# Kernel optimization log

Measured on AMD Instinct MI355X. Metric: run time of the kernel, lower is better.

The kernel has to match this reference:

```python
import jax, jax.numpy as jnp
import numpy as np

B, P, F, E, H, V = 128, 196, 2048, 512, 1024, 10000
TMAX = 30  # max(captions_len) - 1 decode steps
BN_EPS = 1e-5


def setup_inputs() -> dict:
    key = jax.random.key(0)
    ks = jax.random.split(key, 14)
    encoder_feat = jax.random.normal(ks[0], (B, P, F), jnp.float32)
    gt_captions = jax.random.randint(ks[1], (B, TMAX + 1), 0, V, dtype=jnp.int32)
    lens = jax.random.randint(ks[2], (B,), 2, TMAX + 2, dtype=jnp.int32)
    lens = lens.at[0].set(TMAX + 1)
    captions_len = jnp.sort(lens)[::-1]  # sorted descending, as the torch slicing assumes
    embedding = jax.random.uniform(ks[3], (V, E), jnp.float32, -0.1, 0.1)
    W_init = jax.random.normal(ks[4], (E, F), jnp.float32) * np.sqrt(2.0 / F)
    b_init = jnp.zeros((E,), jnp.float32)
    bn_gamma = jnp.ones((E,), jnp.float32)
    bn_beta = jnp.zeros((E,), jnp.float32)
    s = 1.0 / np.sqrt(H)
    W_ih = jax.random.uniform(ks[5], (4 * H, E), jnp.float32, -s, s)
    b_ih = jax.random.uniform(ks[6], (4 * H,), jnp.float32, -s, s)
    W_hh = jax.random.uniform(ks[7], (4 * H, H), jnp.float32, -s, s)
    b_hh = jax.random.uniform(ks[8], (4 * H,), jnp.float32, -s, s)
    W_fc = jax.random.normal(ks[9], (V, H), jnp.float32) * np.sqrt(2.0 / H)
    b_fc = jnp.zeros((V,), jnp.float32)
    return {
        'encoder_feat': encoder_feat, 'gt_captions': gt_captions, 'captions_len': captions_len,
        'embedding': embedding, 'W_init': W_init, 'b_init': b_init,
        'bn_gamma': bn_gamma, 'bn_beta': bn_beta,
        'W_ih': W_ih, 'b_ih': b_ih, 'W_hh': W_hh, 'b_hh': b_hh,
        'W_fc': W_fc, 'b_fc': b_fc,
    }


def _lstm_cell(h, c, x, W_ih, b_ih, W_hh, b_hh):
    # PyTorch LSTMCell: gates = x W_ih^T + b_ih + h W_hh^T + b_hh, order [i, f, g, o]
    gates = x @ W_ih.T + b_ih + h @ W_hh.T + b_hh
    i, f, g, o = jnp.split(gates, 4, axis=-1)
    c_new = jax.nn.sigmoid(f) * c + jax.nn.sigmoid(i) * jnp.tanh(g)
    h_new = jax.nn.sigmoid(o) * jnp.tanh(c_new)
    return h_new, c_new


def reference(encoder_feat, gt_captions, captions_len, embedding, W_init, b_init,
              bn_gamma, bn_beta, W_ih, b_ih, W_hh, b_hh, W_fc, b_fc):
    batch = encoder_feat.shape[0]
    hidden = W_hh.shape[1]
    # t == 0: image feature -> sigmoid(linear) -> BatchNorm1d (eval: rm=0, rv=1)
    feat = encoder_feat.mean(axis=1)                      # [B, F]
    x0 = jax.nn.sigmoid(feat @ W_init.T + b_init)         # [B, E]
    x0 = bn_gamma * (x0 / jnp.sqrt(1.0 + BN_EPS)) + bn_beta
    h0 = jnp.zeros((batch, hidden), x0.dtype)
    c0 = jnp.zeros((batch, hidden), x0.dtype)
    h, c = _lstm_cell(h0, c0, x0, W_ih, b_ih, W_hh, b_hh)
    # decode steps t = 1..TMAX over ground-truth token embeddings
    emb = embedding[gt_captions[:, :TMAX]]                # [B, T, E]
    xs = jnp.swapaxes(emb, 0, 1)                          # [T, B, E]

    def step(carry, x_t):
        h, c = carry
        h, c = _lstm_cell(h, c, x_t, W_ih, b_ih, W_hh, b_hh)
        preds = h @ W_fc.T + b_fc                         # [B, V]
        return (h, c), preds

    _, preds = jax.lax.scan(step, (h, c), xs)             # [T, B, V]
    preds = jnp.swapaxes(preds, 0, 1)                     # [B, T, V]
    # rows beyond batch_size_t were never written in torch (zeros tensor) -> mask
    mask = jnp.arange(TMAX)[None, :] < (captions_len - 1)[:, None]  # [B, T]
    return jnp.where(mask[:, :, None], preds, 0.0)
```

## Files before the change

### kernel.cpp

```cpp
#include <hip/hip_runtime.h>
#include <math.h>

typedef __bf16 bf16;
typedef __bf16 bf16x8 __attribute__((ext_vector_type(8)));
typedef __bf16 bf16x4 __attribute__((ext_vector_type(4)));
typedef float f32x4 __attribute__((ext_vector_type(4)));

#define MFMA_B16(a,b,c) __builtin_amdgcn_mfma_f32_16x16x32_bf16((a),(b),(c),0,0,0)

constexpr int TMAXc = 30;
constexpr int Bc = 128, Pc = 196, Fc = 2048, Ec = 512, Hc = 1024, Vc = 10000;
constexpr int G4c = 4 * Hc;
constexpr int NSTEP = TMAXc + 1;
constexpr int MALLc = NSTEP * Bc;
constexpr int MOUTc = TMAXc * Bc;
constexpr int NBLK = 256;

__device__ __forceinline__ float fsigm(float x){
  return __fdividef(1.0f, 1.0f + __expf(-x));
}
__device__ __forceinline__ float ftanh(float x){
  return 1.0f - __fdividef(2.0f, __expf(2.0f*x) + 1.0f);
}
__device__ __forceinline__ float sel4(float a, float b, float c, float d, int i){
  float x = (i & 1) ? b : a;
  float y = (i & 1) ? d : c;
  return (i & 2) ? y : x;
}

__device__ __forceinline__ void gll16(const void* g, void* l){
  __builtin_amdgcn_global_load_lds((const __attribute__((address_space(1))) void*)g,
                                   (__attribute__((address_space(3))) void*)l, 16, 0, 0);
}

__device__ __forceinline__ void wt16(bf16* p, bf16x8 v){
  asm volatile("global_store_dwordx4 %0, %1, off sc0 sc1" :: "v"(p), "v"(v) : "memory");
}

__device__ __forceinline__ int aldf(int* f){
  return __hip_atomic_load(f, __ATOMIC_RELAXED, __HIP_MEMORY_SCOPE_AGENT);
}

__device__ __forceinline__ void waitflag(int* f, int tgt){
  long long t0 = __builtin_amdgcn_s_memrealtime();
  while (aldf(f) < tgt) {
    __builtin_amdgcn_s_sleep(1);
    if (__builtin_amdgcn_s_memrealtime() - t0 > 100000) break;
  }
}

__device__ __forceinline__ void waitflags4(int* F, int& f1, int& f2, int& f3){
  long long t0 = __builtin_amdgcn_s_memrealtime();
  for (;;) {
    int f0 = aldf(F + 0);
    f1 = aldf(F + 1);
    f2 = aldf(F + 2);
    f3 = aldf(F + 3);
    if (f0 >= 32) break;
    __builtin_amdgcn_s_sleep(1);
    if (__builtin_amdgcn_s_memrealtime() - t0 > 100000) break;
  }
}


__global__ void mean_kernel(const float* __restrict__ enc, bf16* __restrict__ feat){
  int blk = blockIdx.x, b = blk >> 1, half = blk & 1;
  int f0 = half*1024 + threadIdx.x*4;
  const float* p = enc + (size_t)b*Pc*Fc + f0;
  float4 s = {0.f,0.f,0.f,0.f};
  #pragma unroll 4
  for (int q = 0; q < Pc; ++q) {
    float4 v = *(const float4*)(p + (size_t)q*Fc);
    s.x += v.x; s.y += v.y; s.z += v.z; s.w += v.w;
  }
  const float r = 1.0f/(float)Pc;
  bf16x4 o = { (bf16)(s.x*r), (bf16)(s.y*r), (bf16)(s.z*r), (bf16)(s.w*r) };
  *(bf16x4*)&feat[b*Fc + f0] = o;
}

__global__ void conv_kernel(const float* __restrict__ src, bf16* __restrict__ dst, int n4){
  int i = blockIdx.x*256 + threadIdx.x;
  if (i >= n4) return;
  float4 v = ((const float4*)src)[i];
  bf16x4 o = { (bf16)v.x, (bf16)v.y, (bf16)v.z, (bf16)v.w };
  *(bf16x4*)&dst[i*4] = o;
}

__global__ void permconv_ih(const float* __restrict__ W, bf16* __restrict__ Wp){
  int i = blockIdx.x*256 + threadIdx.x;
  if (i >= G4c*Ec/4) return;
  int i4 = i*4;
  int rp = i4 >> 9, k = i4 & 511;
  int g = rp & 3, j = rp >> 2;
  float4 v = *(const float4*)&W[(size_t)(g*Hc + j)*Ec + k];
  bf16x4 o = { (bf16)v.x, (bf16)v.y, (bf16)v.z, (bf16)v.w };
  *(bf16x4*)&Wp[i4] = o;
}

__global__ void permsplit_hh(const float* __restrict__ W, bf16* __restrict__ Whi, bf16* __restrict__ Wlo){
  int i = blockIdx.x*256 + threadIdx.x;
  if (i >= G4c*Hc/4) return;
  int i4 = i*4;
  int rp = i4 >> 10, k = i4 & 1023;
  int g = rp & 3, j = rp >> 2;
  float4 v = *(const float4*)&W[(size_t)(g*Hc + j)*Hc + k];
  bf16 h0=(bf16)v.x, h1=(bf16)v.y, h2=(bf16)v.z, h3=(bf16)v.w;
  bf16x4 hi = { h0, h1, h2, h3 };
  bf16x4 lo = { (bf16)(v.x-(float)h0), (bf16)(v.y-(float)h1), (bf16)(v.z-(float)h2), (bf16)(v.w-(float)h3) };
  *(bf16x4*)&Whi[i4] = hi;
  *(bf16x4*)&Wlo[i4] = lo;
}

__global__ void split_kernel(const float* __restrict__ W, bf16* __restrict__ Whi, bf16* __restrict__ Wlo, int n4){
  int i = blockIdx.x*256 + threadIdx.x;
  if (i >= n4) return;
  float4 v = ((const float4*)W)[i];
  bf16 h0=(bf16)v.x, h1=(bf16)v.y, h2=(bf16)v.z, h3=(bf16)v.w;
  bf16x4 hi = { h0, h1, h2, h3 };
  bf16x4 lo = { (bf16)(v.x-(float)h0), (bf16)(v.y-(float)h1), (bf16)(v.z-(float)h2), (bf16)(v.w-(float)h3) };
  *(bf16x4*)&Whi[i*4] = hi;
  *(bf16x4*)&Wlo[i*4] = lo;
}

__global__ void bcomb_kernel(const float* __restrict__ bih, const float* __restrict__ bhh, float* __restrict__ bc){
  int i = blockIdx.x*256 + threadIdx.x;
  if (i >= G4c) return;
  int g = i & 3, j = i >> 2;
  bc[i] = bih[g*Hc + j] + bhh[g*Hc + j];
}

__global__ void gather_kernel(const float* __restrict__ emb, const int* __restrict__ gt, bf16* __restrict__ X){
  int idx = blockIdx.x*256 + threadIdx.x;
  if (idx >= MOUTc*(Ec/4)) return;
  int r = idx >> 7, ei = (idx & 127) * 4;
  int s = (r >> 7) + 1, b = r & 127;
  int tok = gt[b*(TMAXc+1) + (s-1)];
  float4 v = *(const float4*)(emb + (size_t)tok*Ec + ei);
  bf16x4 o = { (bf16)v.x, (bf16)v.y, (bf16)v.z, (bf16)v.w };
  *(bf16x4*)&X[(size_t)(s*Bc + b)*Ec + ei] = o;
}

__global__ void build_ridx(const int* __restrict__ lens, int* __restrict__ meta){
  int i = blockIdx.x*256 + threadIdx.x;
  if (i >= MOUTc) return;
  int t = i >> 7, b = i & 127;
  int S = 0, R = 0;
  for (int bb = 0; bb < 128; ++bb) {
    int l = lens[bb] - 1;
    S += (t < l) ? t : l;
    R += l;
  }
  if (i == 0) meta[0] = R;
  if (i >= R) meta[1 + i] = 0;
  if (t < lens[b] - 1) meta[1 + S + b] = i;
}

__global__ void zerofill(const int* __restrict__ lens, float* __restrict__ out){
  int i = blockIdx.x*256 + threadIdx.x;
  if (i >= MOUTc*2500) return;
  int row = i / 2500, c4 = i - row*2500;
  int b = row / TMAXc, t = row - b*TMAXc;
  if (t >= lens[b] - 1) {
    float4 z = {0.f,0.f,0.f,0.f};
    *(float4*)(out + (size_t)row*Vc + c4*4) = z;
  }
}

__global__ __launch_bounds__(256, 2) void initA(
  const bf16* __restrict__ feat, const bf16* __restrict__ Wi, float* __restrict__ part)
{
  __shared__ alignas(16) bf16 sA[128*32], sB[128*32];
  int tid = threadIdx.x, lane = tid & 63, w = tid >> 6, wr = w >> 1, wc = w & 1;
  int nt = blockIdx.x & 3, kc = blockIdx.x >> 2;
  int n0 = nt*128;

  f32x4 acc[4][4] = {};
  for (int kt = kc*256; kt < kc*256 + 256; kt += 32) {
    #pragma unroll
    for (int is = 0; is < 2; ++is) {
      int p = tid*16 + is*4096;
      int r = p >> 6, c = (p & 63) >> 1;
      int ldsoff = w*512 + is*2048;
      gll16(feat + (size_t)r*Fc + kt + c, &sA[ldsoff]);
      gll16(Wi + (size_t)(n0 + r)*Fc + kt + c, &sB[ldsoff]);
    }
    __syncthreads();
    int koff = (lane >> 4) * 8;
    bf16x8 ah[4], bh[4];
    #pragma unroll
    for (int mi = 0; mi < 4; ++mi)
      ah[mi] = *(const bf16x8*)&sA[(wr*64 + mi*16 + (lane & 15))*32 + koff];
    #pragma unroll
    for (int ni = 0; ni < 4; ++ni)
      bh[ni] = *(const bf16x8*)&sB[(wc*64 + ni*16 + (lane & 15))*32 + koff];
    #pragma unroll
    for (int mi = 0; mi < 4; ++mi)
      #pragma unroll
      for (int ni = 0; ni < 4; ++ni)
        acc[mi][ni] = MFMA_B16(ah[mi], bh[ni], acc[mi][ni]);
    __syncthreads();
  }
  #pragma unroll
  for (int mi = 0; mi < 4; ++mi)
    #pragma unroll
    for (int ni = 0; ni < 4; ++ni) {
      int lrow = wr*64 + mi*16 + ((lane >> 4) << 2);
      int col = n0 + wc*64 + ni*16 + (lane & 15);
      #pragma unroll
      for (int j = 0; j < 4; ++j)
        part[((size_t)kc*128 + lrow + j)*512 + col] = acc[mi][ni][j];
    }
}

__global__ void initB(const float* __restrict__ part, const float* __restrict__ binit,
                      const float* __restrict__ gam, const float* __restrict__ bet,
                      bf16* __restrict__ Xall)
{
  int i = blockIdx.x*256 + threadIdx.x;
  if (i >= 128*512) return;
  int col = i & 511;
  float v = 0.f;
  #pragma unroll
  for (int kc = 0; kc < 8; ++kc) v += part[(size_t)kc*128*512 + i];
  const float rbn = rsqrtf(1.0f + 1e-5f);
  v = fsigm(v + binit[col]);
  v = gam[col]*(v*rbn) + bet[col];
  Xall[i] = (bf16)v;
}

__global__ __launch_bounds__(256, 2) void gemm_xg(
  const bf16* __restrict__ A, const bf16* __restrict__ B,
  int M, int N, int K, int mtiles,
  const float* __restrict__ p0, bf16* __restrict__ outb)
{
  constexpr int BK = 32;
  __shared__ alignas(16) bf16 sAh[128*BK], sBh[128*BK];

  int tid = threadIdx.x;
  int lane = tid & 63, w = tid >> 6, wr = w >> 1, wc = w & 1;
  int bid = blockIdx.x;
  {
    int nwg = gridDim.x, q = nwg >> 3, r = nwg & 7;
    int x = bid & 7, o = bid >> 3;
    bid = (x < r ? x*(q+1) : r*(q+1) + (x-r)*q) + o;
  }
  int nt = bid / mtiles, mt = bid - nt*mtiles;
  int m0 = mt*128, n0 = nt*128;

  int sr = (tid*16) >> 6;
  int gr0 = m0 + sr, gr1 = m0 + sr + 64;

  f32x4 acc[4][4] = {};

  for (int kt = 0; kt < K; kt += BK) {
    #pragma unroll
    for (int is = 0; is < 2; ++is) {
      int p = tid*16 + is*4096;
      int c = (p & 63) >> 1;
      int r = p >> 6;
      int ldsoff = w*512 + is*2048;
      int ga = is ? gr1 : gr0;
      gll16(A + (size_t)ga*K + kt + c, &sAh[ldsoff]);
      gll16(B + (size_t)(n0 + r)*K + kt + c, &sBh[ldsoff]);
    }
    __syncthreads();

    int koff = (lane >> 4) * 8;
    bf16x8 ah[4], bh[4];
    #pragma unroll
    for (int mi = 0; mi < 4; ++mi)
      ah[mi] = *(const bf16x8*)&sAh[(wr*64 + mi*16 + (lane & 15))*BK + koff];
    #pragma unroll
    for (int ni = 0; ni < 4; ++ni)
      bh[ni] = *(const bf16x8*)&sBh[(wc*64 + ni*16 + (lane & 15))*BK + koff];
    #pragma unroll
    for (int mi = 0; mi < 4; ++mi)
      #pragma unroll
      for (int ni = 0; ni < 4; ++ni)
        acc[mi][ni] = MFMA_B16(ah[mi], bh[ni], acc[mi][ni]);
    __syncthreads();
  }

  #pragma unroll
  for (int mi = 0; mi < 4; ++mi)
    #pragma unroll
    for (int ni = 0; ni < 4; ++ni) {
      int lrow = m0 + wr*64 + mi*16 + ((lane >> 4) << 2);
      int col = n0 + wc*64 + ni*16 + (lane & 15);
      #pragma unroll
      for (int j = 0; j < 4; ++j)
        outb[(size_t)(lrow + j)*G4c + col] = (bf16)(acc[mi][ni][j] + p0[col]);
    }
}


__global__ __launch_bounds__(256, 1) void lstm_persist(
  const bf16* __restrict__ Whi, const bf16* __restrict__ Wlo,
  const bf16* __restrict__ Xg,
  bf16* __restrict__ hCh, bf16* __restrict__ hCl,
  bf16* __restrict__ Hh, bf16* __restrict__ Hl,
  const bf16* __restrict__ WfcHi, const bf16* __restrict__ WfcLo,
  const float* __restrict__ bfc,
  const int* __restrict__ lens, const int* __restrict__ meta,
  float* __restrict__ outf,
  int* __restrict__ flg)
{
  extern __shared__ char sWc[];
  int tid = threadIdx.x, lane = tid & 63, w = tid >> 6;
  int bid = blockIdx.x;
  int strip = bid >> 1, rh = bid & 1;
  int pc0 = strip * 32;
  int row0 = rh * 64 + w * 16;
  int grp = strip >> 5;
  char* scr = sWc + 131072 + w*512;
  int* hallflg = flg + 256;
  int* tilectr = flg + 320;

  for (int ch = tid; ch < 4096; ch += 256) {
    int p = ch >> 7;
    int k = (ch & 127) * 8;
    int ni = p >> 4, bp = p & 15;
    int ks = k >> 5, kg = (k >> 3) & 3;
    int off = (((ks*2 + ni)*4 + kg)*16 + bp) * 16;
    bf16x8 vh = *(const bf16x8*)&Whi[(size_t)(pc0 + p)*Hc + k];
    bf16x8 vl = *(const bf16x8*)&Wlo[(size_t)(pc0 + p)*Hc + k];
    *(bf16x8*)(sWc + off) = vh;
    *(bf16x8*)(sWc + 65536 + off) = vl;
  }
  __syncthreads();

  int bp = lane & 15;
  int bk = (lane >> 4) << 3;
  int rbase = row0 + ((lane >> 4) << 2);
  int e = lane & 3;
  const char* sWhiB = sWc + lane*16;
  const char* sWloB = sWc + 65536 + lane*16;

  int Lh = lens[rh * 64];
  if (Lh > NSTEP) Lh = NSTEP;
  int lenv = lens[row0 + (lane & 15)] - 1;

  float creg[2] = {0.f, 0.f};
  float xgv[2][4];
  #pragma unroll
  for (int ni = 0; ni < 2; ++ni)
    #pragma unroll
    for (int j = 0; j < 4; ++j)
      xgv[ni][j] = (float)Xg[(size_t)(rbase + j)*G4c + pc0 + ni*16 + bp];

#define GATEQ(g, fg) do { if (s > 0) { \
    if (tid == 0 && (fg) < 32) waitflag(&flg[(s*2 + rh)*4 + (g)], 32); \
    __builtin_amdgcn_s_barrier(); \
    asm volatile("" ::: "memory"); } } while (0)

#define LOADQ(qh, ql, g) do { \
    _Pragma("unroll") \
    for (int i = 0; i < 8; ++i) { \
      qh[i] = *(const bf16x8*)(pah + ((g)*8 + i)*32); \
      ql[i] = *(const bf16x8*)(pal + ((g)*8 + i)*32); \
    } \
    asm volatile("" ::: "memory"); } while (0)

#define MFMAQ(qh, ql, g) do { \
    _Pragma("unroll") \
    for (int i = 0; i < 8; ++i) { \
      int ks = (g)*8 + i; \
      _Pragma("unroll") \
      for (int ni = 0; ni < 2; ++ni) { \
        bf16x8 bvh = *(const bf16x8*)(sWhiB + (ks*2 + ni)*1024); \
        bf16x8 bvl = *(const bf16x8*)(sWloB + (ks*2 + ni)*1024); \
        aHH[ni] = MFMA_B16(qh[i], bvh, aHH[ni]); \
        aHL[ni] = MFMA_B16(qh[i], bvl, aHL[ni]); \
        aLH[ni] = MFMA_B16(ql[i], bvh, aLH[ni]); \
      } \
    } } while (0)

  #pragma unroll 1
  for (int s = 0; s < Lh; ++s) {
    const bf16* pah = hCh + (size_t)s*Bc*Hc + (size_t)(row0 + bp)*Hc + bk;
    const bf16* pal = hCl + (size_t)s*Bc*Hc + (size_t)(row0 + bp)*Hc + bk;
    bf16* hwh = hCh + (size_t)(s+1)*Bc*Hc;
    bf16* hwl = hCl + (size_t)(s+1)*Bc*Hc;

    f32x4 aHH[2], aHL[2], aLH[2];
    #pragma unroll
    for (int ni = 0; ni < 2; ++ni) {
      #pragma unroll
      for (int j = 0; j < 4; ++j) aHH[ni][j] = xgv[ni][j];
      aHL[ni] = (f32x4){0.f,0.f,0.f,0.f};
      aLH[ni] = (f32x4){0.f,0.f,0.f,0.f};
    }

    bf16x8 qh0[8], ql0[8], qh1[8], ql1[8];
    int f1 = 32, f2 = 32, f3 = 32;

    if (s > 0) {
      if (tid == 0) waitflags4(&flg[(s*2 + rh)*4], f1, f2, f3);
      __builtin_amdgcn_s_barrier();
      asm volatile("" ::: "memory");
    }
    LOADQ(qh0, ql0, 0);
    GATEQ(1, f1); LOADQ(qh1, ql1, 1);
    MFMAQ(qh0, ql0, 0);
    GATEQ(2, f2); LOADQ(qh0, ql0, 2);
    MFMAQ(qh1, ql1, 1);
    GATEQ(3, f3); LOADQ(qh1, ql1, 3);
    MFMAQ(qh0, ql0, 2);
    MFMAQ(qh1, ql1, 3);

    #pragma unroll
    for (int ni = 0; ni < 2; ++ni) {
      float v0 = aHH[ni][0] + aHL[ni][0] + aLH[ni][0];
      float v1 = aHH[ni][1] + aHL[ni][1] + aLH[ni][1];
      float v2 = aHH[ni][2] + aHL[ni][2] + aLH[ni][2];
      float v3 = aHH[ni][3] + aHL[ni][3] + aLH[ni][3];
      float g0 = sel4(v0, v1, v2, v3, e);
      float g1 = __shfl_xor(sel4(v0, v1, v2, v3, e ^ 1), 1);
      float g2 = __shfl_xor(sel4(v0, v1, v2, v3, e ^ 2), 2);
      float g3 = __shfl_xor(sel4(v0, v1, v2, v3, e ^ 3), 3);
      float gI = sel4(g0, g1, g2, g3, e);
      float gF = sel4(g0, g1, g2, g3, e ^ 1);
      float gG = sel4(g0, g1, g2, g3, e ^ 2);
      float gO = sel4(g0, g1, g2, g3, e ^ 3);

      float co = creg[ni];
      float cn = fsigm(gF)*co + fsigm(gI)*ftanh(gG);
      float hn = fsigm(gO)*ftanh(cn);
      creg[ni] = cn;
      bf16 hhi = (bf16)hn;
      int r16 = ((lane >> 4) << 2) + e;
      int c8  = ni*4 + (bp >> 2);
      *(bf16*)(scr + (r16*8 + c8)*2) = hhi;
      *(bf16*)(scr + 256 + (r16*8 + c8)*2) = (bf16)(hn - (float)hhi);
    }

    asm volatile("s_waitcnt lgkmcnt(0)" ::: "memory");
    __builtin_amdgcn_sched_barrier(0);

    if (lane < 32) {
      int r = lane & 15, buf = lane >> 4;
      bf16x8 vv = *(const bf16x8*)(scr + buf*256 + r*16);
      bf16* dst = (buf ? hwl : hwh) + (size_t)(row0 + r)*Hc + strip*8;
      wt16(dst, vv);
    }

    __syncthreads();
    if (tid == 0 && s + 1 < Lh)
      __hip_atomic_fetch_add(&flg[((s+1)*2 + rh)*4 + grp], 1,
                             __ATOMIC_RELAXED, __HIP_MEMORY_SCOPE_AGENT);

    if (s > 0 && lane >= 32 && (s - 1) < lenv) {
      int r = lane & 15, buf = (lane >> 4) & 1;
      bf16x8 vv = *(const bf16x8*)(scr + buf*256 + r*16);
      wt16((buf ? Hl : Hh) + (size_t)((s-1)*Bc + row0 + r)*Hc + strip*8, vv);
    }
    if (s + 1 < Lh) {
      #pragma unroll
      for (int ni = 0; ni < 2; ++ni)
        #pragma unroll
        for (int j = 0; j < 4; ++j)
          xgv[ni][j] = (float)Xg[(size_t)((s+1)*Bc + rbase + j)*G4c + pc0 + ni*16 + bp];
    }

    __syncthreads();
    if (tid == 0 && s > 0)
      __hip_atomic_fetch_add(&hallflg[(s-1)*2 + rh], 1,
                             __ATOMIC_RELAXED, __HIP_MEMORY_SCOPE_AGENT);
  }
#undef GATEQ
#undef LOADQ
#undef MFMAQ

  if (tid == 0)
    for (int t = Lh - 1; t < TMAXc; ++t)
      __hip_atomic_fetch_add(&hallflg[t*2 + rh], 1,
                             __ATOMIC_RELAXED, __HIP_MEMORY_SCOPE_AGENT);

  __syncthreads();

  bf16* sAh2 = (bf16*)(sWc);
  bf16* sBh2 = (bf16*)(sWc + 32768);
  bf16* sAl2 = (bf16*)(sWc + 65536);
  bf16* sBl2 = (bf16*)(sWc + 98304);
  int* ctrl  = (int*)(sWc + 131072 + 2044);

  int R = meta[0];
  int mtilesFC = (R + 127) >> 7;
  int ntFC = mtilesFC * 79;
  int wr = w >> 1, wc2 = w & 1;

#define STAGE_FC(buf, kt) do { \
    _Pragma("unroll") \
    for (int is = 0; is < 2; ++is) { \
      int p = tid*16 + is*4096; \
      int c = (p & 63) >> 1; \
      int r = p >> 6; \
      int ldsoff = (buf)*4096 + w*512 + is*2048; \
      int ga = is ? gr1 : gr0; \
      int rb = n0 + r; if (rb > 9999) rb = 9999; \
      gll16(Hh + (size_t)ga*Hc + (kt) + c, &sAh2[ldsoff]); \
      gll16(WfcHi + (size_t)rb*Hc + (kt) + c, &sBh2[ldsoff]); \
      gll16(Hl + (size_t)ga*Hc + (kt) + c, &sAl2[ldsoff]); \
      gll16(WfcLo + (size_t)rb*Hc + (kt) + c, &sBl2[ldsoff]); \
    } } while (0)

  #pragma unroll 1
  for (;;) {
    if (tid == 0) ctrl[0] = __hip_atomic_fetch_add(tilectr, 1,
                               __ATOMIC_RELAXED, __HIP_MEMORY_SCOPE_AGENT);
    __syncthreads();
    int idx = ctrl[0];
    __syncthreads();
    if (idx >= ntFC) break;
    int mt = idx / 79, ntc = idx - mt*79;
    int m0 = mt*128, n0 = ntc*128;
    int last = m0 + 127; if (last >= R) last = R - 1;
    int tmax = meta[1 + last] >> 7;
    if (tid == 0) {
      waitflag(&hallflg[tmax*2 + 0], 128);
      waitflag(&hallflg[tmax*2 + 1], 128);
    }
    __builtin_amdgcn_s_barrier();
    asm volatile("" ::: "memory");

    int sr = (tid*16) >> 6;
    int gr0 = meta[1 + m0 + sr], gr1 = meta[1 + m0 + sr + 64];

    f32x4 acc[4][4] = {};

    STAGE_FC(0, 0);
    asm volatile("s_waitcnt vmcnt(0)" ::: "memory");
    __builtin_amdgcn_s_barrier();
    asm volatile("" ::: "memory");

    #pragma unroll 1
    for (int ks = 0; ks < 32; ++ks) {
      int buf = ks & 1;
      if (ks + 1 < 32) STAGE_FC(buf ^ 1, (ks+1)*32);

      int koff = (lane >> 4) * 8;
      int bb = buf*4096;
      bf16x8 ah[4], bh[4], al[4], bl[4];
      #pragma unroll
      for (int mi = 0; mi < 4; ++mi) {
        int rr = wr*64 + mi*16 + (lane & 15);
        ah[mi] = *(const bf16x8*)&sAh2[bb + rr*32 + koff];
        al[mi] = *(const bf16x8*)&sAl2[bb + rr*32 + koff];
      }
      #pragma unroll
      for (int ni = 0; ni < 4; ++ni) {
        int rr = wc2*64 + ni*16 + (lane & 15);
        bh[ni] = *(const bf16x8*)&sBh2[bb + rr*32 + koff];
        bl[ni] = *(const bf16x8*)&sBl2[bb + rr*32 + koff];
      }
      #pragma unroll
      for (int mi = 0; mi < 4; ++mi)
        #pragma unroll
        for (int ni = 0; ni < 4; ++ni) {
          acc[mi][ni] = MFMA_B16(ah[mi], bh[ni], acc[mi][ni]);
          acc[mi][ni] = MFMA_B16(ah[mi], bl[ni], acc[mi][ni]);
          acc[mi][ni] = MFMA_B16(al[mi], bh[ni], acc[mi][ni]);
        }

      asm volatile("s_waitcnt vmcnt(0)" ::: "memory");
      __builtin_amdgcn_s_barrier();
      asm volatile("" ::: "memory");
    }

    #pragma unroll
    for (int mi = 0; mi < 4; ++mi)
      #pragma unroll
      for (int ni = 0; ni < 4; ++ni) {
        int lrow = m0 + wr*64 + mi*16 + ((lane >> 4) << 2);
        int col = n0 + wc2*64 + ni*16 + (lane & 15);
        #pragma unroll
        for (int j = 0; j < 4; ++j) {
          int rr = lrow + j;
          if (rr < R && col < Vc) {
            int val = meta[1 + rr];
            int t = val >> 7, b = val & 127;
            outf[(size_t)b*(TMAXc*Vc) + (size_t)t*Vc + col] = acc[mi][ni][j] + bfc[col];
          }
        }
      }
  }
#undef STAGE_FC
}


extern "C" void kernel_launch(void* const* d_in, const int* in_sizes, int n_in,
                              void* d_out, int out_size, void* d_ws, size_t ws_size,
                              hipStream_t stream)
{
  const float* enc   = (const float*)d_in[0];
  const int*   gt    = (const int*)  d_in[1];
  const int*   lens  = (const int*)  d_in[2];
  const float* emb   = (const float*)d_in[3];
  const float* Winit = (const float*)d_in[4];
  const float* binit = (const float*)d_in[5];
  const float* gam   = (const float*)d_in[6];
  const float* bet   = (const float*)d_in[7];
  const float* Wih   = (const float*)d_in[8];
  const float* bih   = (const float*)d_in[9];
  const float* Whh   = (const float*)d_in[10];
  const float* bhh   = (const float*)d_in[11];
  const float* Wfc   = (const float*)d_in[12];
  const float* bfc   = (const float*)d_in[13];
  float* out = (float*)d_out;

  char* ws = (char*)d_ws;
  size_t off = 0;
  auto alloc = [&](size_t bytes) -> char* {
    char* p = ws + off;
    off += (bytes + 255) & ~(size_t)255;
    return p;
  };

  bf16* featB  = (bf16*)alloc((size_t)Bc*Fc*2);
  bf16* WinitB = (bf16*)alloc((size_t)Ec*Fc*2);
  bf16* WihpB  = (bf16*)alloc((size_t)G4c*Ec*2);
  bf16* WhhHi  = (bf16*)alloc((size_t)G4c*Hc*2);
  bf16* WhhLo  = (bf16*)alloc((size_t)G4c*Hc*2);
  bf16* WfcHi  = (bf16*)alloc((size_t)Vc*Hc*2);
  bf16* WfcLo  = (bf16*)alloc((size_t)Vc*Hc*2);
  float* bcomb = (float*)alloc((size_t)G4c*4);
  bf16* Xall   = (bf16*)alloc((size_t)MALLc*Ec*2);
  bf16* Xg     = (bf16*)alloc((size_t)MALLc*G4c*2);
  bf16* hChH   = (bf16*)alloc((size_t)(NSTEP+1)*Bc*Hc*2);
  bf16* hChL   = (bf16*)alloc((size_t)(NSTEP+1)*Bc*Hc*2);
  bf16* HallH  = (bf16*)alloc((size_t)MOUTc*Hc*2);
  bf16* HallL  = (bf16*)alloc((size_t)MOUTc*Hc*2);
  float* part  = (float*)alloc((size_t)8*128*512*4);
  int*  meta   = (int*) alloc((size_t)(1 + MOUTc)*4);
  int*  flg    = (int*) alloc((size_t)384*4);

  if (off > ws_size) return;

  hipMemsetAsync(hChH, 0, (size_t)Bc*Hc*2, stream);
  hipMemsetAsync(hChL, 0, (size_t)Bc*Hc*2, stream);
  hipMemsetAsync(flg, 0, (size_t)384*4, stream);

  mean_kernel<<<256, 256, 0, stream>>>(enc, featB);
  conv_kernel<<<(Ec*Fc/4 + 255)/256, 256, 0, stream>>>(Winit, WinitB, Ec*Fc/4);
  permconv_ih<<<(G4c*Ec/4 + 255)/256, 256, 0, stream>>>(Wih, WihpB);
  permsplit_hh<<<(G4c*Hc/4 + 255)/256, 256, 0, stream>>>(Whh, WhhHi, WhhLo);
  split_kernel<<<(Vc*Hc/4 + 255)/256, 256, 0, stream>>>(Wfc, WfcHi, WfcLo, Vc*Hc/4);
  bcomb_kernel<<<(G4c + 255)/256, 256, 0, stream>>>(bih, bhh, bcomb);
  gather_kernel<<<(MOUTc*(Ec/4) + 255)/256, 256, 0, stream>>>(emb, gt, Xall);
  build_ridx<<<(MOUTc + 255)/256, 256, 0, stream>>>(lens, meta);
  zerofill<<<(MOUTc*2500 + 255)/256, 256, 0, stream>>>(lens, out);

  initA<<<32, 256, 0, stream>>>(featB, WinitB, part);
  initB<<<(128*512 + 255)/256, 256, 0, stream>>>(part, binit, gam, bet, Xall);

  gemm_xg<<<31*32, 256, 0, stream>>>(
      Xall, WihpB, MALLc, G4c, Ec, 31, bcomb, Xg);

  hipFuncSetAttribute(reinterpret_cast<const void*>(lstm_persist),
                      hipFuncAttributeMaxDynamicSharedMemorySize, 133120);
  lstm_persist<<<NBLK, 256, 133120, stream>>>(
      WhhHi, WhhLo, Xg, hChH, hChL, HallH, HallL,
      WfcHi, WfcLo, bfc, lens, meta, out, flg);
}
```

Before: 653.0 us.

## Deepen FC GEMM staging to 4-buffer ring and drop a per-step LSTM barrier

The vocabulary-projection GEMM now uses a four-slot LDS ring with three K-slices in flight and partial vmcnt waits, replacing the double buffer that fully drained global loads every iteration. The recurrent loop also drops its second __syncthreads per step and publishes the hidden-state-ready flag one step later, with the final flag emitted after the loop. This is meant to hide global-load latency in the FC tiles and cut barrier overhead in the serial LSTM loop. In exchange the flag signalling is delayed a step and vmcnt counts must match the exact number of issued loads.

```diff
diff --git a/kernel.cpp b/kernel.cpp
--- a/kernel.cpp
+++ b/kernel.cpp
@@ -445,9 +445,14 @@
     }
 
     __syncthreads();
-    if (tid == 0 && s + 1 < Lh)
-      __hip_atomic_fetch_add(&flg[((s+1)*2 + rh)*4 + grp], 1,
-                             __ATOMIC_RELAXED, __HIP_MEMORY_SCOPE_AGENT);
+    if (tid == 0) {
+      if (s + 1 < Lh)
+        __hip_atomic_fetch_add(&flg[((s+1)*2 + rh)*4 + grp], 1,
+                               __ATOMIC_RELAXED, __HIP_MEMORY_SCOPE_AGENT);
+      if (s >= 2)
+        __hip_atomic_fetch_add(&hallflg[(s-2)*2 + rh], 1,
+                               __ATOMIC_RELAXED, __HIP_MEMORY_SCOPE_AGENT);
+    }
 
     if (s > 0 && lane >= 32 && (s - 1) < lenv) {
       int r = lane & 15, buf = (lane >> 4) & 1;
@@ -461,47 +466,42 @@
         for (int j = 0; j < 4; ++j)
           xgv[ni][j] = (float)Xg[(size_t)((s+1)*Bc + rbase + j)*G4c + pc0 + ni*16 + bp];
     }
-
-    __syncthreads();
-    if (tid == 0 && s > 0)
-      __hip_atomic_fetch_add(&hallflg[(s-1)*2 + rh], 1,
-                             __ATOMIC_RELAXED, __HIP_MEMORY_SCOPE_AGENT);
   }
 #undef GATEQ
 #undef LOADQ
 #undef MFMAQ
 
-  if (tid == 0)
+  __syncthreads();
+  if (tid == 0) {
+    if (Lh >= 2)
+      __hip_atomic_fetch_add(&hallflg[(Lh-2)*2 + rh], 1,
+                             __ATOMIC_RELAXED, __HIP_MEMORY_SCOPE_AGENT);
     for (int t = Lh - 1; t < TMAXc; ++t)
       __hip_atomic_fetch_add(&hallflg[t*2 + rh], 1,
                              __ATOMIC_RELAXED, __HIP_MEMORY_SCOPE_AGENT);
-
-  __syncthreads();
-
-  bf16* sAh2 = (bf16*)(sWc);
-  bf16* sBh2 = (bf16*)(sWc + 32768);
-  bf16* sAl2 = (bf16*)(sWc + 65536);
-  bf16* sBl2 = (bf16*)(sWc + 98304);
-  int* ctrl  = (int*)(sWc + 131072 + 2044);
+  }
+
+  bf16* L = (bf16*)sWc;
+  int* ctrl = (int*)(sWc + 131072 + 2044);
 
   int R = meta[0];
   int mtilesFC = (R + 127) >> 7;
   int ntFC = mtilesFC * 79;
   int wr = w >> 1, wc2 = w & 1;
 
-#define STAGE_FC(buf, kt) do { \
+#define STAGE_FC(bufb, kt) do { \
     _Pragma("unroll") \
     for (int is = 0; is < 2; ++is) { \
       int p = tid*16 + is*4096; \
       int c = (p & 63) >> 1; \
       int r = p >> 6; \
-      int ldsoff = (buf)*4096 + w*512 + is*2048; \
+      int eo = (bufb)*16384 + w*512 + is*2048; \
       int ga = is ? gr1 : gr0; \
       int rb = n0 + r; if (rb > 9999) rb = 9999; \
-      gll16(Hh + (size_t)ga*Hc + (kt) + c, &sAh2[ldsoff]); \
-      gll16(WfcHi + (size_t)rb*Hc + (kt) + c, &sBh2[ldsoff]); \
-      gll16(Hl + (size_t)ga*Hc + (kt) + c, &sAl2[ldsoff]); \
-      gll16(WfcLo + (size_t)rb*Hc + (kt) + c, &sBl2[ldsoff]); \
+      gll16(Hh + (size_t)ga*Hc + (kt) + c, L + eo); \
+      gll16(WfcHi + (size_t)rb*Hc + (kt) + c, L + 4096 + eo); \
+      gll16(Hl + (size_t)ga*Hc + (kt) + c, L + 8192 + eo); \
+      gll16(WfcLo + (size_t)rb*Hc + (kt) + c, L + 12288 + eo); \
     } } while (0)
 
   #pragma unroll 1
@@ -529,29 +529,32 @@
     f32x4 acc[4][4] = {};
 
     STAGE_FC(0, 0);
-    asm volatile("s_waitcnt vmcnt(0)" ::: "memory");
-    __builtin_amdgcn_s_barrier();
-    asm volatile("" ::: "memory");
+    STAGE_FC(1, 32);
+    STAGE_FC(2, 64);
 
     #pragma unroll 1
     for (int ks = 0; ks < 32; ++ks) {
-      int buf = ks & 1;
-      if (ks + 1 < 32) STAGE_FC(buf ^ 1, (ks+1)*32);
+      if (ks <= 29)      asm volatile("s_waitcnt vmcnt(16)" ::: "memory");
+      else if (ks == 30) asm volatile("s_waitcnt vmcnt(8)"  ::: "memory");
+      else               asm volatile("s_waitcnt vmcnt(0)"  ::: "memory");
+      __builtin_amdgcn_s_barrier();
+      asm volatile("" ::: "memory");
+      if (ks + 3 < 32) STAGE_FC((ks+3) & 3, (ks+3)*32);
 
       int koff = (lane >> 4) * 8;
-      int bb = buf*4096;
+      int bb = (ks & 3) * 16384;
       bf16x8 ah[4], bh[4], al[4], bl[4];
       #pragma unroll
       for (int mi = 0; mi < 4; ++mi) {
         int rr = wr*64 + mi*16 + (lane & 15);
-        ah[mi] = *(const bf16x8*)&sAh2[bb + rr*32 + koff];
-        al[mi] = *(const bf16x8*)&sAl2[bb + rr*32 + koff];
+        ah[mi] = *(const bf16x8*)&L[bb + rr*32 + koff];
+        al[mi] = *(const bf16x8*)&L[bb + 8192 + rr*32 + koff];
       }
       #pragma unroll
       for (int ni = 0; ni < 4; ++ni) {
         int rr = wc2*64 + ni*16 + (lane & 15);
-        bh[ni] = *(const bf16x8*)&sBh2[bb + rr*32 + koff];
-        bl[ni] = *(const bf16x8*)&sBl2[bb + rr*32 + koff];
+        bh[ni] = *(const bf16x8*)&L[bb + 4096 + rr*32 + koff];
+        bl[ni] = *(const bf16x8*)&L[bb + 12288 + rr*32 + koff];
       }
       #pragma unroll
       for (int mi = 0; mi < 4; ++mi)
@@ -561,10 +564,6 @@
           acc[mi][ni] = MFMA_B16(ah[mi], bl[ni], acc[mi][ni]);
           acc[mi][ni] = MFMA_B16(al[mi], bh[ni], acc[mi][ni]);
         }
-
-      asm volatile("s_waitcnt vmcnt(0)" ::: "memory");
-      __builtin_amdgcn_s_barrier();
-      asm volatile("" ::: "memory");
     }
 
     #pragma unroll
```

New measurement: 619.6 us. 5.1% less time.
